# Performance work log

Measured on AMD Instinct MI355X. Metric: run time of the kernel, lower is better.

The kernel has to match this reference:

```python
import jax, jax.numpy as jnp
import numpy as np

N, E, C, F = 20000, 320000, 64, 8
DIN = 2 * C + F + 1           # MLP input: sender scalars + receiver scalars + radial feats + length
AVG = 16.0                    # avg_num_neighbors
INV_SQRT3 = 0.5773502691896258


def setup_inputs() -> dict:
    key = jax.random.key(0)
    ks = jax.random.split(key, 16)
    d = {}
    d["node_feats"] = jax.random.normal(ks[0], (N, C + 3 * C), jnp.float32)  # 64x0e + 64x1o (mul-major)
    d["edge_attrs"] = jax.random.normal(ks[1], (E, 4), jnp.float32)           # SH: 1x0e + 1x1o
    d["edge_feats"] = jax.random.normal(ks[2], (E, F), jnp.float32)           # radial basis
    d["lengths"] = jax.random.uniform(ks[3], (E, 1), jnp.float32)
    d["edge_index"] = jax.random.randint(ks[4], (2, E), 0, N, jnp.int32)      # (sender, receiver)
    d["Wsc"] = jax.random.normal(ks[5], (C, C), jnp.float32) / np.sqrt(C).astype(np.float32)
    d["Wup0"] = jax.random.normal(ks[6], (C, C), jnp.float32) / np.sqrt(C).astype(np.float32)
    d["Wup1"] = jax.random.normal(ks[7], (C, C), jnp.float32) / np.sqrt(C).astype(np.float32)
    d["W1"] = jax.random.normal(ks[8], (DIN, C), jnp.float32) / np.sqrt(DIN).astype(np.float32)
    d["b1"] = jnp.zeros((C,), jnp.float32)
    d["W2"] = jax.random.normal(ks[9], (C, C), jnp.float32) / np.sqrt(C).astype(np.float32)
    d["b2"] = jnp.zeros((C,), jnp.float32)
    d["W3"] = jax.random.normal(ks[10], (C, 4 * C), jnp.float32) * 1e-3       # near-zero init like the source
    d["Ws"] = jax.random.normal(ks[11], (2 * C, C), jnp.float32) / np.sqrt(2 * C).astype(np.float32)
    d["Wv"] = jax.random.normal(ks[12], (2 * C, C), jnp.float32) / np.sqrt(2 * C).astype(np.float32)
    return d


def reference(node_feats, edge_attrs, edge_feats, lengths, edge_index,
              Wsc, Wup0, Wup1, W1, b1, W2, b2, W3, Ws, Wv):
    n = node_feats.shape[0]
    s = node_feats[:, :C]                          # [N,C] scalar (0e) channels
    v = node_feats[:, C:].reshape(n, C, 3)         # [N,C,3] vector (1o) channels

    node_scalars = s @ Wsc                          # linear_scalar -> 64x0e
    s_up = s @ Wup0                                 # linear_up, 0e block
    v_up = jnp.einsum('nci,cd->ndi', v, Wup1)       # linear_up, 1o block

    snd, rcv = edge_index[0], edge_index[1]

    # weight MLP: Dense->silu->Dense->silu->Dense(no bias)
    mlp_in = jnp.concatenate([node_scalars[snd], node_scalars[rcv], edge_feats, lengths], axis=-1)
    h = jax.nn.silu(mlp_in @ W1 + b1)
    h = jax.nn.silu(h @ W2 + b2)
    tw = h @ W3                                     # [E, 4C] per-irrep tp weights
    w0, w1, w2, w3 = jnp.split(tw, 4, axis=-1)

    y0 = edge_attrs[:, :1]                          # [E,1] SH l=0
    y1 = edge_attrs[:, 1:4]                         # [E,3] SH l=1
    xs = s_up[snd]                                  # [E,C]   gather senders
    xv = v_up[snd]                                  # [E,C,3]

    # weighted tensor product paths (component normalization), filtered to 0e/1o
    p0 = xs * y0 * w0                                               # 0e x 0e -> 0e  [E,C]
    p1 = (jnp.einsum('eci,ei->ec', xv, y1) * INV_SQRT3) * w1        # 1o x 1o -> 0e  [E,C]
    p2 = xs[:, :, None] * y1[:, None, :] * w2[:, :, None]           # 0e x 1o -> 1o  [E,C,3]
    p3 = xv * y0[:, :, None] * w3[:, :, None]                       # 1o x 0e -> 1o  [E,C,3]

    # scatter_sum messages into receiver nodes
    m0 = jax.ops.segment_sum(jnp.concatenate([p0, p1], axis=-1), rcv, num_segments=n)  # [N,2C]
    m1 = jax.ops.segment_sum(jnp.concatenate([p2, p3], axis=1), rcv, num_segments=n)   # [N,2C,3]

    # final equivariant linear on simplified irreps_mid (128x0e + 128x1o), / avg_num_neighbors
    out_s = (m0 @ Ws) / AVG                          # [N,C]
    out_v = jnp.einsum('nci,cd->ndi', m1, Wv) / AVG  # [N,C,3]

    # reshape_irreps -> [N, channels, 1 + 3]
    return jnp.concatenate([out_s[:, :, None], out_v], axis=-1)
```

## Files before the change

### kernel.cpp

```cpp
#include <hip/hip_runtime.h>

#define N_NODES 20000
#define N_EDGES 320000
#define INV_SQRT3 0.5773502691896258f

typedef unsigned short u16;
typedef unsigned int u32;
typedef __attribute__((ext_vector_type(8))) short short8;
typedef __attribute__((ext_vector_type(4))) float f32x4;
typedef __attribute__((ext_vector_type(4))) u32 u32x4v;

static const size_t OFF_NSBF = 0;
static const size_t OFF_SV   = 2560000;
static const size_t OFF_MG   = 23040000;
static const size_t OFF_TW   = 64000000;
static const size_t OFF_W1F  = 227840000;
static const size_t OFF_W2F  = 227860480;
static const size_t OFF_W3F  = 227868672;
static const size_t OFF_WNF  = 227901440;
static const size_t OFF_CNT  = 227950592;
static const size_t OFF_OFFS = 228030592;
static const size_t OFF_CUR  = 228110608;
static const size_t OFF_ES   = 228190608;
static const size_t OFF_SS   = 229470608;
static const size_t OFF_RS   = 230750608;

static __device__ __forceinline__ u16 f2bf(float x) {
    union { float f; u32 u; } c; c.f = x;
    u32 u = c.u + 0x7fffu + ((c.u >> 16) & 1u);
    return (u16)(u >> 16);
}
static __device__ __forceinline__ float bf2f(u16 b) {
    union { u32 u; float f; } c; c.u = (u32)b << 16; return c.f;
}
static __device__ __forceinline__ u16 f2h(float x) {
    union { _Float16 h; u16 u; } c; c.h = (_Float16)x; return c.u;
}
static __device__ __forceinline__ float h2f(u32 b) {
    union { u16 u; _Float16 h; } c; c.u = (u16)b; return (float)c.h;
}
static __device__ __forceinline__ f32x4 mfma16(short8 a, short8 b, f32x4 c) {
    return __builtin_amdgcn_mfma_f32_16x16x32_bf16(a, b, c, 0, 0, 0);
}
static __device__ __forceinline__ float silu(float x) {
    return x / (1.0f + __expf(-x));
}
template <typename T>
static __device__ __forceinline__ T ntload(const T* p) { return __builtin_nontemporal_load(p); }
template <typename T>
static __device__ __forceinline__ void ntstore(T* p, T v) { __builtin_nontemporal_store(v, p); }

__global__ void prep_w_kernel(const float* __restrict__ W1, const float* __restrict__ W2,
                              const float* __restrict__ W3,
                              u16* __restrict__ W1f, u16* __restrict__ W2f, u16* __restrict__ W3f) {
    int t = blockIdx.x * 256 + threadIdx.x;
    if (t >= 3840) return;
    int l = t & 63, grp = t >> 6;
    int hi = l >> 4, lo = l & 15;
    if (grp < 20) {
        int kk = grp >> 2, jt = grp & 3;
#pragma unroll
        for (int e2 = 0; e2 < 8; e2++) {
            int k = kk * 32 + hi * 8 + e2, j = jt * 16 + lo;
            W1f[(size_t)(grp * 64 + l) * 8 + e2] = (k < 137) ? f2bf(W1[k * 64 + j]) : (u16)0;
        }
    } else if (grp < 28) {
        int g = grp - 20; int kk = g >> 2, jt = g & 3;
#pragma unroll
        for (int e2 = 0; e2 < 8; e2++) {
            int k = kk * 32 + hi * 8 + e2, j = jt * 16 + lo;
            W2f[(size_t)(g * 64 + l) * 8 + e2] = f2bf(W2[k * 64 + j]);
        }
    } else {
        int g = grp - 28; int kk = g >> 4, jt = g & 15;
#pragma unroll
        for (int e2 = 0; e2 < 8; e2++) {
            int k = kk * 32 + hi * 8 + e2, j = jt * 16 + lo;
            W3f[(size_t)(g * 64 + l) * 8 + e2] = f2bf(W3[k * 256 + j]);
        }
    }
}

__global__ void prep_wn_kernel(const float* __restrict__ Wsc, const float* __restrict__ Wup0,
                               const float* __restrict__ Wup1, u16* __restrict__ WNF) {
    int t = blockIdx.x * 256 + threadIdx.x;
    if (t >= 1536) return;
    int mat = t >> 9;
    int rem = t & 511;
    int g = rem >> 6, l = rem & 63;
    int kk = g >> 2, jt = g & 3, hi = l >> 4, lo = l & 15;
    const float* W = (mat == 0) ? Wsc : (mat == 1) ? Wup0 : Wup1;
    u16* dh = WNF + (size_t)mat * 8192 + (size_t)(g * 64 + l) * 8;
    u16* dl = dh + 4096;
#pragma unroll
    for (int e2 = 0; e2 < 8; e2++) {
        int k = kk * 32 + hi * 8 + e2, d = jt * 16 + lo;
        float w = W[k * 64 + d];
        u16 h = f2bf(w);
        dh[e2] = h;
        dl[e2] = f2bf(w - bf2f(h));
    }
}

__global__ void prep_w2_kernel(const float* __restrict__ Ws, const float* __restrict__ Wv,
                               u16* __restrict__ WSF) {
    int t = blockIdx.x * 256 + threadIdx.x;
    if (t >= 2048) return;
    int l = t & 63, grp = t >> 6;
    int wsel = grp >> 4;
    int g = grp & 15;
    int kk = g >> 2, jt = g & 3;
    int hi = l >> 4, lo = l & 15;
    const float* W = wsel ? Wv : Ws;
    u16* dh = WSF + (size_t)wsel * 16384;
    u16* dl = dh + 8192;
    size_t base = (size_t)(g * 64 + l) * 8;
#pragma unroll
    for (int e2 = 0; e2 < 8; e2++) {
        int k = kk * 32 + hi * 8 + e2, d = jt * 16 + lo;
        float w = W[k * 64 + d];
        u16 h = f2bf(w);
        float r = w - bf2f(h);
        dh[base + e2] = h;
        dl[base + e2] = f2bf(r);
    }
}

__global__ __launch_bounds__(256) void node_prep_kernel(
    const float* __restrict__ node_feats, const u16* __restrict__ WNF,
    u16* __restrict__ ns_bf, f32x4* __restrict__ sv) {
    const int tid = threadIdx.x;
    const int lane = tid & 63;
    const int w = tid >> 6;
    const int lo16 = lane & 15;
    const int hi = lane >> 4;
    const int nb = blockIdx.x * 64 + w * 16;

    int an = nb + lo16; if (an > N_NODES - 1) an = N_NODES - 1;
    const float* arow = node_feats + (size_t)an * 256;

    const short8* B = (const short8*)WNF;

    f32x4 acc_ns[4], acc_su[4], acc_v[3][4];
#pragma unroll
    for (int jt = 0; jt < 4; jt++) {
        acc_ns[jt] = (f32x4)(0.0f);
        acc_su[jt] = (f32x4)(0.0f);
#pragma unroll
        for (int i = 0; i < 3; i++) acc_v[i][jt] = (f32x4)(0.0f);
    }

#pragma unroll
    for (int kk = 0; kk < 2; kk++) {
        short8 sh, sl;
        {
            const float* sp = arow + kk * 32 + hi * 8;
            f32x4 x0 = *(const f32x4*)sp;
            f32x4 x1 = *(const f32x4*)(sp + 4);
#pragma unroll
            for (int j = 0; j < 4; j++) {
                u16 h0 = f2bf(x0[j]);
                sh[j] = (short)h0;
                sl[j] = (short)f2bf(x0[j] - bf2f(h0));
                u16 h1 = f2bf(x1[j]);
                sh[4 + j] = (short)h1;
                sl[4 + j] = (short)f2bf(x1[j] - bf2f(h1));
            }
        }
        short8 vh[3], vl[3];
#pragma unroll
        for (int i = 0; i < 3; i++) {
            const float* vp = arow + 64 + i + 3 * (kk * 32 + hi * 8);
#pragma unroll
            for (int e = 0; e < 8; e++) {
                float x = vp[e * 3];
                u16 hb = f2bf(x);
                vh[i][e] = (short)hb;
                vl[i][e] = (short)f2bf(x - bf2f(hb));
            }
        }
#pragma unroll
        for (int jt = 0; jt < 4; jt++) {
            int fi = (kk * 4 + jt) * 64 + lane;
            short8 bh = B[fi], bl = B[512 + fi];
            acc_ns[jt] = mfma16(sh, bh, acc_ns[jt]);
            acc_ns[jt] = mfma16(sl, bh, acc_ns[jt]);
            acc_ns[jt] = mfma16(sh, bl, acc_ns[jt]);
            bh = B[1024 + fi]; bl = B[1536 + fi];
            acc_su[jt] = mfma16(sh, bh, acc_su[jt]);
            acc_su[jt] = mfma16(sl, bh, acc_su[jt]);
            acc_su[jt] = mfma16(sh, bl, acc_su[jt]);
            bh = B[2048 + fi]; bl = B[2560 + fi];
#pragma unroll
            for (int i = 0; i < 3; i++) {
                acc_v[i][jt] = mfma16(vh[i], bh, acc_v[i][jt]);
                acc_v[i][jt] = mfma16(vl[i], bh, acc_v[i][jt]);
                acc_v[i][jt] = mfma16(vh[i], bl, acc_v[i][jt]);
            }
        }
    }

#pragma unroll
    for (int r = 0; r < 4; r++) {
        int n = nb + hi * 4 + r;
        if (n < N_NODES) {
#pragma unroll
            for (int jt = 0; jt < 4; jt++) {
                int d = jt * 16 + lo16;
                ns_bf[(size_t)n * 64 + d] = f2bf(acc_ns[jt][r]);
                f32x4 o;
                o.x = acc_su[jt][r];
                o.y = acc_v[0][jt][r];
                o.z = acc_v[1][jt][r];
                o.w = acc_v[2][jt][r];
                sv[(size_t)n * 64 + d] = o;
            }
        }
    }
}

__global__ void hist_kernel(const int* __restrict__ ei, int* __restrict__ cnt) {
    int e = blockIdx.x * 256 + threadIdx.x;
    if (e < N_EDGES) atomicAdd(&cnt[ei[N_EDGES + e]], 1);
}

__global__ void scan_kernel(const int* __restrict__ cnt, int* __restrict__ offs,
                            int* __restrict__ cursor) {
    __shared__ int buf[1024];
    int t = threadIdx.x;
    int base = t * 20;
    int loc[20];
    int tot = 0;
    int v20[20];
    if (base < N_NODES) {
#pragma unroll
        for (int q = 0; q < 5; q++) {
            int4 vv = *(const int4*)&cnt[base + q * 4];
            v20[q * 4 + 0] = vv.x; v20[q * 4 + 1] = vv.y;
            v20[q * 4 + 2] = vv.z; v20[q * 4 + 3] = vv.w;
        }
    } else {
#pragma unroll
        for (int i = 0; i < 20; i++) v20[i] = 0;
    }
#pragma unroll
    for (int i = 0; i < 20; i++) { loc[i] = tot; tot += v20[i]; }
    buf[t] = tot;
    __syncthreads();
    for (int d = 1; d < 1024; d <<= 1) {
        int add = (t >= d) ? buf[t - d] : 0;
        __syncthreads();
        buf[t] += add;
        __syncthreads();
    }
    int ebase = buf[t] - tot;
#pragma unroll
    for (int i = 0; i < 20; i++) {
        int idx = base + i;
        if (idx < N_NODES) { int o = ebase + loc[i]; offs[idx] = o; cursor[idx] = o; }
    }
    if (t == 1023) offs[N_NODES] = buf[1023];
}

__global__ void scatter_kernel(const int* __restrict__ ei, int* __restrict__ cursor,
                               int* __restrict__ esort, int* __restrict__ ssort,
                               int* __restrict__ rsort) {
    int e = blockIdx.x * 256 + threadIdx.x;
    if (e < N_EDGES) {
        int sn = ei[e];
        int rc = ei[N_EDGES + e];
        int pos = atomicAdd(&cursor[rc], 1);
        esort[pos] = e;
        ssort[pos] = sn;
        rsort[pos] = rc;
    }
}

__global__ __launch_bounds__(256, 5) void mlp_kernel(
    const u16* __restrict__ ns_bf,
    const u16* __restrict__ W1f, const u16* __restrict__ W2f, const u16* __restrict__ W3f,
    const float* __restrict__ b1, const float* __restrict__ b2,
    const float* __restrict__ edge_feats, const float* __restrict__ lengths,
    const int* __restrict__ esort, const int* __restrict__ ssort, const int* __restrict__ rsort,
    u16* __restrict__ twg) {

    __shared__ u16 mlpbuf[64][168];
    __shared__ u16 h1s[64][72];
    u16* h2sf = &mlpbuf[0][0];

    const int tid = threadIdx.x;
    const int l = tid & 63;
    const int lo16 = l & 15;
    const int hi = l >> 4;
    const int w = tid >> 6;
    const int erow = (w << 4) | lo16;
    const int koff = hi * 8;
    const int drow = (w << 4) + hi * 4;

    const int p0 = blockIdx.x * 64;

    const short8* w1frag = (const short8*)W1f;
    const short8* w2frag = (const short8*)W2f;
    const short8* w3frag = (const short8*)W3f;

    float bb1[4], bb2[4];
#pragma unroll
    for (int jt = 0; jt < 4; jt++) { bb1[jt] = b1[jt * 16 + lo16]; bb2[jt] = b2[jt * 16 + lo16]; }

    {
        int rr = tid >> 2, pp = tid & 3;
        uint4 z = {0, 0, 0, 0};
        *(uint4*)&mlpbuf[rr][136 + pp * 8] = z;
    }

    {
        int es = tid >> 2, part = tid & 3;
        int e = esort[p0 + es];
        int sn = ssort[p0 + es];
        int rc = rsort[p0 + es];
        const uint4* ps = (const uint4*)(ns_bf + (size_t)sn * 64 + part * 16);
        uint4 s0 = ps[0], s1 = ps[1];
        *(uint4*)&mlpbuf[es][part * 16] = s0;
        *(uint4*)&mlpbuf[es][part * 16 + 8] = s1;
        const uint4* pr = (const uint4*)(ns_bf + (size_t)rc * 64 + part * 16);
        uint4 r0v = pr[0], r1v = pr[1];
        *(uint4*)&mlpbuf[es][64 + part * 16] = r0v;
        *(uint4*)&mlpbuf[es][64 + part * 16 + 8] = r1v;
        if (part == 0) {
            float4 f0 = *(const float4*)(edge_feats + (size_t)e * 8);
            float4 f1 = *(const float4*)(edge_feats + (size_t)e * 8 + 4);
            u32 pk0 = (u32)f2bf(f0.x) | ((u32)f2bf(f0.y) << 16);
            u32 pk1 = (u32)f2bf(f0.z) | ((u32)f2bf(f0.w) << 16);
            u32 pk2 = (u32)f2bf(f1.x) | ((u32)f2bf(f1.y) << 16);
            u32 pk3 = (u32)f2bf(f1.z) | ((u32)f2bf(f1.w) << 16);
            uint4 pk = {pk0, pk1, pk2, pk3};
            *(uint4*)&mlpbuf[es][128] = pk;
            mlpbuf[es][136] = f2bf(lengths[e]);
        }
    }
    __syncthreads();

    f32x4 a1c[4];
#pragma unroll
    for (int jt = 0; jt < 4; jt++) a1c[jt] = (f32x4)(0.0f);
#pragma unroll
    for (int kk = 0; kk < 5; kk++) {
        short8 af = *(const short8*)&mlpbuf[erow][kk * 32 + koff];
        const short8* wb = w1frag + kk * 256 + l;
        a1c[0] = mfma16(af, wb[0],   a1c[0]);
        a1c[1] = mfma16(af, wb[64],  a1c[1]);
        a1c[2] = mfma16(af, wb[128], a1c[2]);
        a1c[3] = mfma16(af, wb[192], a1c[3]);
    }
#pragma unroll
    for (int jt = 0; jt < 4; jt++) {
#pragma unroll
        for (int r = 0; r < 4; r++) {
            float x = a1c[jt][r] + bb1[jt];
            h1s[drow + r][jt * 16 + lo16] = f2bf(silu(x));
        }
    }
    __syncthreads();

    f32x4 a2c[4];
#pragma unroll
    for (int jt = 0; jt < 4; jt++) a2c[jt] = (f32x4)(0.0f);
#pragma unroll
    for (int kk = 0; kk < 2; kk++) {
        short8 af = *(const short8*)&h1s[erow][kk * 32 + koff];
        const short8* wb = w2frag + kk * 256 + l;
        a2c[0] = mfma16(af, wb[0],   a2c[0]);
        a2c[1] = mfma16(af, wb[64],  a2c[1]);
        a2c[2] = mfma16(af, wb[128], a2c[2]);
        a2c[3] = mfma16(af, wb[192], a2c[3]);
    }
#pragma unroll
    for (int jt = 0; jt < 4; jt++) {
#pragma unroll
        for (int r = 0; r < 4; r++) {
            float x = a2c[jt][r] + bb2[jt];
            h2sf[(drow + r) * 72 + jt * 16 + lo16] = f2bf(silu(x));
        }
    }
    __syncthreads();

    f32x4 tw[16];
#pragma unroll
    for (int jt = 0; jt < 16; jt++) tw[jt] = (f32x4)(0.0f);
#pragma unroll
    for (int kk = 0; kk < 2; kk++) {
        short8 af = *(const short8*)&h2sf[erow * 72 + kk * 32 + koff];
        const short8* wb = w3frag + kk * 1024 + l;
#pragma unroll
        for (int jt = 0; jt < 16; jt++) tw[jt] = mfma16(af, wb[jt * 64], tw[jt]);
    }

    int relrow = p0 + drow;
#pragma unroll
    for (int r = 0; r < 4; r++) {
        u32 q0a = (u32)f2h(tw[0][r])  | ((u32)f2h(tw[1][r])  << 16);
        u32 q0b = (u32)f2h(tw[2][r])  | ((u32)f2h(tw[3][r])  << 16);
        u32 q1a = (u32)f2h(tw[4][r])  | ((u32)f2h(tw[5][r])  << 16);
        u32 q1b = (u32)f2h(tw[6][r])  | ((u32)f2h(tw[7][r])  << 16);
        u32 q2a = (u32)f2h(tw[8][r])  | ((u32)f2h(tw[9][r])  << 16);
        u32 q2b = (u32)f2h(tw[10][r]) | ((u32)f2h(tw[11][r]) << 16);
        u32 q3a = (u32)f2h(tw[12][r]) | ((u32)f2h(tw[13][r]) << 16);
        u32 q3b = (u32)f2h(tw[14][r]) | ((u32)f2h(tw[15][r]) << 16);
        u16* dst = twg + (size_t)(relrow + r) * 256 + lo16 * 16;
        u32x4v A = {q0a, q0b, q1a, q1b};
        u32x4v B = {q2a, q2b, q3a, q3b};
        *(u32x4v*)dst = A;
        *(((u32x4v*)dst) + 1) = B;
    }
}

__global__ __launch_bounds__(256, 4) void seg_kernel(
    const f32x4* __restrict__ sv, const float* __restrict__ edge_attrs,
    const int* __restrict__ esort, const int* __restrict__ ssort,
    const int* __restrict__ offs, const u16* __restrict__ twg,
    float* __restrict__ m_g) {
    const int lane = threadIdx.x & 63;
    const int wv = threadIdx.x >> 6;
    const int n = blockIdx.x * 4 + wv;
    const int c = lane;
    const int jt = c >> 4, lo16 = c & 15;
    const int e0 = offs[n], e1 = offs[n + 1];
    float a_m0 = 0.f, a_m0b = 0.f;
    float a20 = 0.f, a21 = 0.f, a22 = 0.f, a30 = 0.f, a31 = 0.f, a32 = 0.f;
#pragma unroll 4
    for (int pos = e0; pos < e1; ++pos) {
        int e = esort[pos];
        int sn = ssort[pos];
        const u16* twp = twg + (size_t)pos * 256 + lo16 * 16;
        u32x4v ta = *((const u32x4v*)twp);
        u32x4v tb = *(((const u32x4v*)twp) + 1);
        f32x4 y4 = *(const f32x4*)(edge_attrs + (size_t)e * 4);
        f32x4 s4 = sv[(size_t)sn * 64 + c];
        u32 wwa = (jt & 2) ? ta.y : ta.x;
        u32 wwb = (jt & 2) ? ta.w : ta.z;
        u32 wwc = (jt & 2) ? tb.y : tb.x;
        u32 wwd = (jt & 2) ? tb.w : tb.z;
        int sh = (jt & 1) << 4;
        float w0 = h2f((wwa >> sh) & 0xffffu);
        float w1 = h2f((wwb >> sh) & 0xffffu);
        float w2 = h2f((wwc >> sh) & 0xffffu);
        float w3 = h2f((wwd >> sh) & 0xffffu);
        float xs = s4.x, xv0 = s4.y, xv1 = s4.z, xv2 = s4.w;
        float y0 = y4.x, ya = y4.y, yb = y4.z, yc = y4.w;
        a_m0 = fmaf(xs * y0, w0, a_m0);
        float dv = xv0 * ya + xv1 * yb + xv2 * yc;
        a_m0b = fmaf(dv, w1, a_m0b);
        float sw2 = xs * w2;
        a20 = fmaf(sw2, ya, a20); a21 = fmaf(sw2, yb, a21); a22 = fmaf(sw2, yc, a22);
        float yw3 = y0 * w3;
        a30 = fmaf(xv0, yw3, a30); a31 = fmaf(xv1, yw3, a31); a32 = fmaf(xv2, yw3, a32);
    }
    float* mr = m_g + (size_t)n * 512;
    ntstore(mr + c,        a_m0);
    ntstore(mr + 64 + c,   a_m0b * INV_SQRT3);
    ntstore(mr + 128 + c,  a20);
    ntstore(mr + 192 + c,  a30);
    ntstore(mr + 256 + c,  a21);
    ntstore(mr + 320 + c,  a31);
    ntstore(mr + 384 + c,  a22);
    ntstore(mr + 448 + c,  a32);
}

__global__ __launch_bounds__(256, 2) void out_kernel(
    const float* __restrict__ m_g, const u16* __restrict__ WSF,
    float* __restrict__ out) {
    const int tid = threadIdx.x;
    const int lane = tid & 63;
    const int w = tid >> 6;
    const int lo16 = lane & 15;
    const int hi = lane >> 4;
    const int nb = blockIdx.x * 64 + w * 16;

    int arow_n = nb + lo16;
    if (arow_n > N_NODES - 1) arow_n = N_NODES - 1;
    const float* arow = m_g + (size_t)arow_n * 512 + hi * 8;

    const short8* bsh = (const short8*)WSF;
    const short8* bsl = (const short8*)(WSF + 8192);
    const short8* bvh = (const short8*)(WSF + 16384);
    const short8* bvl = (const short8*)(WSF + 24576);

    f32x4 acc[4][4];
#pragma unroll
    for (int q = 0; q < 4; q++)
#pragma unroll
        for (int jt = 0; jt < 4; jt++) acc[q][jt] = (f32x4)(0.0f);

#pragma unroll
    for (int kk = 0; kk < 4; kk++) {
        short8 ahi[4], alo[4];
#pragma unroll
        for (int q = 0; q < 4; q++) {
            const float* p = arow + q * 128 + kk * 32;
            f32x4 x0 = ntload((const f32x4*)p);
            f32x4 x1 = ntload((const f32x4*)(p + 4));
#pragma unroll
            for (int j = 0; j < 4; j++) {
                u16 h0 = f2bf(x0[j]);
                ahi[q][j] = (short)h0;
                alo[q][j] = (short)f2bf(x0[j] - bf2f(h0));
                u16 h1 = f2bf(x1[j]);
                ahi[q][4 + j] = (short)h1;
                alo[q][4 + j] = (short)f2bf(x1[j] - bf2f(h1));
            }
        }
#pragma unroll
        for (int jt = 0; jt < 4; jt++) {
            int bidx = (kk * 4 + jt) * 64 + lane;
            short8 wh_s = bsh[bidx];
            short8 wl_s = bsl[bidx];
            short8 wh_v = bvh[bidx];
            short8 wl_v = bvl[bidx];
            acc[0][jt] = mfma16(ahi[0], wh_s, acc[0][jt]);
            acc[0][jt] = mfma16(alo[0], wh_s, acc[0][jt]);
            acc[0][jt] = mfma16(ahi[0], wl_s, acc[0][jt]);
#pragma unroll
            for (int q = 1; q < 4; q++) {
                acc[q][jt] = mfma16(ahi[q], wh_v, acc[q][jt]);
                acc[q][jt] = mfma16(alo[q], wh_v, acc[q][jt]);
                acc[q][jt] = mfma16(ahi[q], wl_v, acc[q][jt]);
            }
        }
    }

#pragma unroll
    for (int r = 0; r < 4; r++) {
        int n = nb + hi * 4 + r;
        if (n < N_NODES) {
#pragma unroll
            for (int jt = 0; jt < 4; jt++) {
                int d = jt * 16 + lo16;
                f32x4 o;
                o.x = acc[0][jt][r] * 0.0625f;
                o.y = acc[1][jt][r] * 0.0625f;
                o.z = acc[2][jt][r] * 0.0625f;
                o.w = acc[3][jt][r] * 0.0625f;
                ntstore((f32x4*)(out + (size_t)n * 256 + d * 4), o);
            }
        }
    }
}

extern "C" void kernel_launch(void* const* d_in, const int* in_sizes, int n_in,
                              void* d_out, int out_size, void* d_ws, size_t ws_size,
                              hipStream_t stream) {
    (void)in_sizes; (void)n_in; (void)out_size; (void)ws_size;
    const float* node_feats = (const float*)d_in[0];
    const float* edge_attrs = (const float*)d_in[1];
    const float* edge_feats = (const float*)d_in[2];
    const float* lengths    = (const float*)d_in[3];
    const int*   edge_index = (const int*)d_in[4];
    const float* Wsc  = (const float*)d_in[5];
    const float* Wup0 = (const float*)d_in[6];
    const float* Wup1 = (const float*)d_in[7];
    const float* W1   = (const float*)d_in[8];
    const float* b1   = (const float*)d_in[9];
    const float* W2   = (const float*)d_in[10];
    const float* b2   = (const float*)d_in[11];
    const float* W3   = (const float*)d_in[12];
    const float* Ws   = (const float*)d_in[13];
    const float* Wv   = (const float*)d_in[14];

    char* ws = (char*)d_ws;
    u16*   ns_bf  = (u16*)(ws + OFF_NSBF);
    f32x4* sv     = (f32x4*)(ws + OFF_SV);
    float* m_g    = (float*)(ws + OFF_MG);
    u16*   twg    = (u16*)(ws + OFF_TW);
    u16*   W1f    = (u16*)(ws + OFF_W1F);
    u16*   W2f    = (u16*)(ws + OFF_W2F);
    u16*   W3f    = (u16*)(ws + OFF_W3F);
    u16*   WNF    = (u16*)(ws + OFF_WNF);
    int*   cnt    = (int*)(ws + OFF_CNT);
    int*   offs   = (int*)(ws + OFF_OFFS);
    int*   cursor = (int*)(ws + OFF_CUR);
    u16*   WSF    = (u16*)(ws + OFF_CUR);
    int*   esort  = (int*)(ws + OFF_ES);
    int*   ssort  = (int*)(ws + OFF_SS);
    int*   rsort  = (int*)(ws + OFF_RS);
    float* out    = (float*)d_out;

    (void)hipMemsetAsync(cnt, 0, N_NODES * sizeof(int), stream);
    prep_w_kernel<<<15, 256, 0, stream>>>(W1, W2, W3, W1f, W2f, W3f);
    prep_wn_kernel<<<6, 256, 0, stream>>>(Wsc, Wup0, Wup1, WNF);
    node_prep_kernel<<<(N_NODES + 63) / 64, 256, 0, stream>>>(node_feats, WNF, ns_bf, sv);
    hist_kernel<<<N_EDGES / 256, 256, 0, stream>>>(edge_index, cnt);
    scan_kernel<<<1, 1024, 0, stream>>>(cnt, offs, cursor);
    scatter_kernel<<<N_EDGES / 256, 256, 0, stream>>>(edge_index, cursor, esort, ssort, rsort);
    prep_w2_kernel<<<8, 256, 0, stream>>>(Ws, Wv, WSF);

    mlp_kernel<<<N_EDGES / 64, 256, 0, stream>>>(ns_bf, W1f, W2f, W3f, b1, b2,
                                                 edge_feats, lengths,
                                                 esort, ssort, rsort, twg);
    seg_kernel<<<N_NODES / 4, 256, 0, stream>>>(sv, edge_attrs, esort, ssort,
                                                offs, twg, m_g);
    out_kernel<<<(N_NODES + 63) / 64, 256, 0, stream>>>(m_g, WSF, out);
}
```

Baseline: 268.3 us.

## Store node features in fp16, pre-sort edge attrs, switch MLP layers 2-3 to f16

```diff
diff --git a/kernel.cpp b/kernel.cpp
--- a/kernel.cpp
+++ b/kernel.cpp
@@ -7,6 +7,8 @@
 typedef unsigned short u16;
 typedef unsigned int u32;
 typedef __attribute__((ext_vector_type(8))) short short8;
+typedef __attribute__((ext_vector_type(8))) _Float16 half8;
+typedef __attribute__((ext_vector_type(2))) __fp16 fp16x2;
 typedef __attribute__((ext_vector_type(4))) float f32x4;
 typedef __attribute__((ext_vector_type(4))) u32 u32x4v;
 
@@ -24,6 +26,7 @@
 static const size_t OFF_ES   = 228190608;
 static const size_t OFF_SS   = 229470608;
 static const size_t OFF_RS   = 230750608;
+static const size_t OFF_EA   = 232030608;
 
 static __device__ __forceinline__ u16 f2bf(float x) {
     union { float f; u32 u; } c; c.f = x;
@@ -39,8 +42,16 @@
 static __device__ __forceinline__ float h2f(u32 b) {
     union { u16 u; _Float16 h; } c; c.u = (u16)b; return (float)c.h;
 }
+static __device__ __forceinline__ u32 pkh(float a, float b) {
+    union { fp16x2 h; u32 u; } c;
+    c.h = __builtin_amdgcn_cvt_pkrtz(a, b);
+    return c.u;
+}
 static __device__ __forceinline__ f32x4 mfma16(short8 a, short8 b, f32x4 c) {
     return __builtin_amdgcn_mfma_f32_16x16x32_bf16(a, b, c, 0, 0, 0);
+}
+static __device__ __forceinline__ f32x4 mfma16h(half8 a, half8 b, f32x4 c) {
+    return __builtin_amdgcn_mfma_f32_16x16x32_f16(a, b, c, 0, 0, 0);
 }
 static __device__ __forceinline__ float silu(float x) {
     return x / (1.0f + __expf(-x));
@@ -69,14 +80,16 @@
 #pragma unroll
         for (int e2 = 0; e2 < 8; e2++) {
             int k = kk * 32 + hi * 8 + e2, j = jt * 16 + lo;
-            W2f[(size_t)(g * 64 + l) * 8 + e2] = f2bf(W2[k * 64 + j]);
+            int kp = ((k & 3) << 4) + (k >> 2);
+            W2f[(size_t)(g * 64 + l) * 8 + e2] = f2h(W2[kp * 64 + j]);
         }
     } else {
         int g = grp - 28; int kk = g >> 4, jt = g & 15;
 #pragma unroll
         for (int e2 = 0; e2 < 8; e2++) {
             int k = kk * 32 + hi * 8 + e2, j = jt * 16 + lo;
-            W3f[(size_t)(g * 64 + l) * 8 + e2] = f2bf(W3[k * 256 + j]);
+            int kp = ((k & 3) << 4) + (k >> 2);
+            W3f[(size_t)(g * 64 + l) * 8 + e2] = f2h(W3[kp * 256 + j]);
         }
     }
 }
@@ -128,7 +141,7 @@
 
 __global__ __launch_bounds__(256) void node_prep_kernel(
     const float* __restrict__ node_feats, const u16* __restrict__ WNF,
-    u16* __restrict__ ns_bf, f32x4* __restrict__ sv) {
+    u16* __restrict__ ns_bf, u16* __restrict__ svh) {
     const int tid = threadIdx.x;
     const int lane = tid & 63;
     const int w = tid >> 6;
@@ -208,12 +221,10 @@
             for (int jt = 0; jt < 4; jt++) {
                 int d = jt * 16 + lo16;
                 ns_bf[(size_t)n * 64 + d] = f2bf(acc_ns[jt][r]);
-                f32x4 o;
-                o.x = acc_su[jt][r];
-                o.y = acc_v[0][jt][r];
-                o.z = acc_v[1][jt][r];
-                o.w = acc_v[2][jt][r];
-                sv[(size_t)n * 64 + d] = o;
+                uint2 o;
+                o.x = pkh(acc_su[jt][r], acc_v[0][jt][r]);
+                o.y = pkh(acc_v[1][jt][r], acc_v[2][jt][r]);
+                *(uint2*)&svh[((size_t)n * 64 + d) * 4] = o;
             }
         }
     }
@@ -262,17 +273,20 @@
     if (t == 1023) offs[N_NODES] = buf[1023];
 }
 
-__global__ void scatter_kernel(const int* __restrict__ ei, int* __restrict__ cursor,
+__global__ void scatter_kernel(const int* __restrict__ ei, const float* __restrict__ edge_attrs,
+                               int* __restrict__ cursor,
                                int* __restrict__ esort, int* __restrict__ ssort,
-                               int* __restrict__ rsort) {
+                               int* __restrict__ rsort, float* __restrict__ easort) {
     int e = blockIdx.x * 256 + threadIdx.x;
     if (e < N_EDGES) {
         int sn = ei[e];
         int rc = ei[N_EDGES + e];
+        float4 ea = *(const float4*)(edge_attrs + (size_t)e * 4);
         int pos = atomicAdd(&cursor[rc], 1);
         esort[pos] = e;
         ssort[pos] = sn;
         rsort[pos] = rc;
+        *(float4*)(easort + (size_t)pos * 4) = ea;
     }
 }
 
@@ -300,8 +314,8 @@
     const int p0 = blockIdx.x * 64;
 
     const short8* w1frag = (const short8*)W1f;
-    const short8* w2frag = (const short8*)W2f;
-    const short8* w3frag = (const short8*)W3f;
+    const half8* w2frag = (const half8*)W2f;
+    const half8* w3frag = (const half8*)W3f;
 
     float bb1[4], bb2[4];
 #pragma unroll
@@ -353,12 +367,11 @@
         a1c[3] = mfma16(af, wb[192], a1c[3]);
     }
 #pragma unroll
-    for (int jt = 0; jt < 4; jt++) {
-#pragma unroll
-        for (int r = 0; r < 4; r++) {
-            float x = a1c[jt][r] + bb1[jt];
-            h1s[drow + r][jt * 16 + lo16] = f2bf(silu(x));
-        }
+    for (int r = 0; r < 4; r++) {
+        uint2 pk;
+        pk.x = pkh(silu(a1c[0][r] + bb1[0]), silu(a1c[1][r] + bb1[1]));
+        pk.y = pkh(silu(a1c[2][r] + bb1[2]), silu(a1c[3][r] + bb1[3]));
+        *(uint2*)&h1s[drow + r][lo16 * 4] = pk;
     }
     __syncthreads();
 
@@ -367,20 +380,19 @@
     for (int jt = 0; jt < 4; jt++) a2c[jt] = (f32x4)(0.0f);
 #pragma unroll
     for (int kk = 0; kk < 2; kk++) {
-        short8 af = *(const short8*)&h1s[erow][kk * 32 + koff];
-        const short8* wb = w2frag + kk * 256 + l;
-        a2c[0] = mfma16(af, wb[0],   a2c[0]);
-        a2c[1] = mfma16(af, wb[64],  a2c[1]);
-        a2c[2] = mfma16(af, wb[128], a2c[2]);
-        a2c[3] = mfma16(af, wb[192], a2c[3]);
-    }
-#pragma unroll
-    for (int jt = 0; jt < 4; jt++) {
-#pragma unroll
-        for (int r = 0; r < 4; r++) {
-            float x = a2c[jt][r] + bb2[jt];
-            h2sf[(drow + r) * 72 + jt * 16 + lo16] = f2bf(silu(x));
-        }
+        half8 af = *(const half8*)&h1s[erow][kk * 32 + koff];
+        const half8* wb = w2frag + kk * 256 + l;
+        a2c[0] = mfma16h(af, wb[0],   a2c[0]);
+        a2c[1] = mfma16h(af, wb[64],  a2c[1]);
+        a2c[2] = mfma16h(af, wb[128], a2c[2]);
+        a2c[3] = mfma16h(af, wb[192], a2c[3]);
+    }
+#pragma unroll
+    for (int r = 0; r < 4; r++) {
+        uint2 pk;
+        pk.x = pkh(silu(a2c[0][r] + bb2[0]), silu(a2c[1][r] + bb2[1]));
+        pk.y = pkh(silu(a2c[2][r] + bb2[2]), silu(a2c[3][r] + bb2[3]));
+        *(uint2*)&h2sf[(drow + r) * 72 + lo16 * 4] = pk;
     }
     __syncthreads();
 
@@ -389,34 +401,33 @@
     for (int jt = 0; jt < 16; jt++) tw[jt] = (f32x4)(0.0f);
 #pragma unroll
     for (int kk = 0; kk < 2; kk++) {
-        short8 af = *(const short8*)&h2sf[erow * 72 + kk * 32 + koff];
-        const short8* wb = w3frag + kk * 1024 + l;
-#pragma unroll
-        for (int jt = 0; jt < 16; jt++) tw[jt] = mfma16(af, wb[jt * 64], tw[jt]);
+        half8 af = *(const half8*)&h2sf[erow * 72 + kk * 32 + koff];
+        const half8* wb = w3frag + kk * 1024 + l;
+#pragma unroll
+        for (int jt = 0; jt < 16; jt++) tw[jt] = mfma16h(af, wb[jt * 64], tw[jt]);
     }
 
     int relrow = p0 + drow;
 #pragma unroll
     for (int r = 0; r < 4; r++) {
-        u32 q0a = (u32)f2h(tw[0][r])  | ((u32)f2h(tw[1][r])  << 16);
-        u32 q0b = (u32)f2h(tw[2][r])  | ((u32)f2h(tw[3][r])  << 16);
-        u32 q1a = (u32)f2h(tw[4][r])  | ((u32)f2h(tw[5][r])  << 16);
-        u32 q1b = (u32)f2h(tw[6][r])  | ((u32)f2h(tw[7][r])  << 16);
-        u32 q2a = (u32)f2h(tw[8][r])  | ((u32)f2h(tw[9][r])  << 16);
-        u32 q2b = (u32)f2h(tw[10][r]) | ((u32)f2h(tw[11][r]) << 16);
-        u32 q3a = (u32)f2h(tw[12][r]) | ((u32)f2h(tw[13][r]) << 16);
-        u32 q3b = (u32)f2h(tw[14][r]) | ((u32)f2h(tw[15][r]) << 16);
+        u32x4v A, B;
+        A.x = pkh(tw[0][r],  tw[1][r]);
+        A.y = pkh(tw[2][r],  tw[3][r]);
+        A.z = pkh(tw[4][r],  tw[5][r]);
+        A.w = pkh(tw[6][r],  tw[7][r]);
+        B.x = pkh(tw[8][r],  tw[9][r]);
+        B.y = pkh(tw[10][r], tw[11][r]);
+        B.z = pkh(tw[12][r], tw[13][r]);
+        B.w = pkh(tw[14][r], tw[15][r]);
         u16* dst = twg + (size_t)(relrow + r) * 256 + lo16 * 16;
-        u32x4v A = {q0a, q0b, q1a, q1b};
-        u32x4v B = {q2a, q2b, q3a, q3b};
         *(u32x4v*)dst = A;
         *(((u32x4v*)dst) + 1) = B;
     }
 }
 
 __global__ __launch_bounds__(256, 4) void seg_kernel(
-    const f32x4* __restrict__ sv, const float* __restrict__ edge_attrs,
-    const int* __restrict__ esort, const int* __restrict__ ssort,
+    const u16* __restrict__ svh, const float* __restrict__ easort,
+    const int* __restrict__ ssort,
     const int* __restrict__ offs, const u16* __restrict__ twg,
     float* __restrict__ m_g) {
     const int lane = threadIdx.x & 63;
@@ -429,13 +440,12 @@
     float a20 = 0.f, a21 = 0.f, a22 = 0.f, a30 = 0.f, a31 = 0.f, a32 = 0.f;
 #pragma unroll 4
     for (int pos = e0; pos < e1; ++pos) {
-        int e = esort[pos];
         int sn = ssort[pos];
         const u16* twp = twg + (size_t)pos * 256 + lo16 * 16;
         u32x4v ta = *((const u32x4v*)twp);
         u32x4v tb = *(((const u32x4v*)twp) + 1);
-        f32x4 y4 = *(const f32x4*)(edge_attrs + (size_t)e * 4);
-        f32x4 s4 = sv[(size_t)sn * 64 + c];
+        f32x4 y4 = *(const f32x4*)(easort + (size_t)pos * 4);
+        uint2 sp = *(const uint2*)&svh[((size_t)sn * 64 + c) * 4];
         u32 wwa = (jt & 2) ? ta.y : ta.x;
         u32 wwb = (jt & 2) ? ta.w : ta.z;
         u32 wwc = (jt & 2) ? tb.y : tb.x;
@@ -445,7 +455,10 @@
         float w1 = h2f((wwb >> sh) & 0xffffu);
         float w2 = h2f((wwc >> sh) & 0xffffu);
         float w3 = h2f((wwd >> sh) & 0xffffu);
-        float xs = s4.x, xv0 = s4.y, xv1 = s4.z, xv2 = s4.w;
+        float xs  = h2f(sp.x & 0xffffu);
+        float xv0 = h2f(sp.x >> 16);
+        float xv1 = h2f(sp.y & 0xffffu);
+        float xv2 = h2f(sp.y >> 16);
         float y0 = y4.x, ya = y4.y, yb = y4.z, yc = y4.w;
         a_m0 = fmaf(xs * y0, w0, a_m0);
         float dv = xv0 * ya + xv1 * yb + xv2 * yc;
@@ -568,7 +581,7 @@
 
     char* ws = (char*)d_ws;
     u16*   ns_bf  = (u16*)(ws + OFF_NSBF);
-    f32x4* sv     = (f32x4*)(ws + OFF_SV);
+    u16*   svh    = (u16*)(ws + OFF_SV);
     float* m_g    = (float*)(ws + OFF_MG);
     u16*   twg    = (u16*)(ws + OFF_TW);
     u16*   W1f    = (u16*)(ws + OFF_W1F);
@@ -582,21 +595,23 @@
     int*   esort  = (int*)(ws + OFF_ES);
     int*   ssort  = (int*)(ws + OFF_SS);
     int*   rsort  = (int*)(ws + OFF_RS);
+    float* easort = (float*)(ws + OFF_EA);
     float* out    = (float*)d_out;
 
     (void)hipMemsetAsync(cnt, 0, N_NODES * sizeof(int), stream);
     prep_w_kernel<<<15, 256, 0, stream>>>(W1, W2, W3, W1f, W2f, W3f);
     prep_wn_kernel<<<6, 256, 0, stream>>>(Wsc, Wup0, Wup1, WNF);
-    node_prep_kernel<<<(N_NODES + 63) / 64, 256, 0, stream>>>(node_feats, WNF, ns_bf, sv);
+    node_prep_kernel<<<(N_NODES + 63) / 64, 256, 0, stream>>>(node_feats, WNF, ns_bf, svh);
     hist_kernel<<<N_EDGES / 256, 256, 0, stream>>>(edge_index, cnt);
     scan_kernel<<<1, 1024, 0, stream>>>(cnt, offs, cursor);
-    scatter_kernel<<<N_EDGES / 256, 256, 0, stream>>>(edge_index, cursor, esort, ssort, rsort);
+    scatter_kernel<<<N_EDGES / 256, 256, 0, stream>>>(edge_index, edge_attrs, cursor,
+                                                      esort, ssort, rsort, easort);
     prep_w2_kernel<<<8, 256, 0, stream>>>(Ws, Wv, WSF);
 
     mlp_kernel<<<N_EDGES / 64, 256, 0, stream>>>(ns_bf, W1f, W2f, W3f, b1, b2,
                                                  edge_feats, lengths,
                                                  esort, ssort, rsort, twg);
-    seg_kernel<<<N_NODES / 4, 256, 0, stream>>>(sv, edge_attrs, esort, ssort,
+    seg_kernel<<<N_NODES / 4, 256, 0, stream>>>(svh, easort, ssort,
                                                 offs, twg, m_g);
     out_kernel<<<(N_NODES + 63) / 64, 256, 0, stream>>>(m_g, WSF, out);
 }
```

Result: faster. 247.0 us (-7.9%).
